# Optimization experiments

Hardware: AMD Instinct MI355X
Metric: run time of the kernel (lower is better)

Reference implementation:

```python
import jax, jax.numpy as jnp
import numpy as np

P = 1024
H = 256
W = 256


def setup_inputs() -> dict:
    key = jax.random.key(0)
    k1, k2, k3, k4, k5, k6 = jax.random.split(key, 6)
    # Means in pixel coordinates, inside the image
    means_2d = jax.random.uniform(k1, (P, 2), dtype=jnp.float32) * jnp.array([W, H], dtype=jnp.float32)
    # Symmetric positive-definite 2x2 covariances packed as (a, b, c) = (cxx, cxy, cyy)
    a = 5.0 + 20.0 * jax.random.uniform(k2, (P,), dtype=jnp.float32)
    c = 5.0 + 20.0 * jax.random.uniform(k3, (P,), dtype=jnp.float32)
    b = (jax.random.uniform(k4, (P,), dtype=jnp.float32) - 0.5) * jnp.sqrt(a * c)  # |b| < 0.5*sqrt(ac) => det > 0
    covs_2d = jnp.stack([a, b, c], axis=-1)
    depth_features = 0.1 + 10.0 * jax.random.uniform(k5, (P,), dtype=jnp.float32)
    color_features = jax.random.uniform(k6, (P, 3), dtype=jnp.float32)
    return {
        "means_2d": means_2d,
        "covs_2d": covs_2d,
        "depth_features": depth_features,
        "color_features": color_features,
        "height": H,
        "width": W,
    }


def reference(means_2d, covs_2d, depth_features, color_features, height, width):
    # Front-to-back ordering by depth (nearest Gaussian composited first)
    order = jnp.argsort(depth_features)
    means = means_2d[order]          # [P,2]
    covs = covs_2d[order]            # [P,3]
    colors = color_features[order]   # [P,3]

    a, b, c = covs[:, 0], covs[:, 1], covs[:, 2]
    det = a * c - b * b
    ia = c / det
    ib = -b / det
    ic = a / det

    xs = jnp.arange(width, dtype=means.dtype) + 0.5   # pixel centers
    ys = jnp.arange(height, dtype=means.dtype) + 0.5
    dx = xs[None, None, :] - means[:, 0][:, None, None]   # [P,1,W]
    dy = ys[None, :, None] - means[:, 1][:, None, None]   # [P,H,1]

    # Mahalanobis distance under inverse 2D covariance (conic)
    q = (ia[:, None, None] * dx * dx
         + 2.0 * ib[:, None, None] * dx * dy
         + ic[:, None, None] * dy * dy)                   # [P,H,W]

    alpha = jnp.minimum(0.99, jnp.exp(-0.5 * q))
    alpha = jnp.where(alpha < 1.0 / 255.0, 0.0, alpha)    # 3DGS skip threshold

    # Exclusive cumulative transmittance along the depth-sorted axis
    T = jnp.cumprod(1.0 - alpha, axis=0)                  # [P,H,W]
    T_excl = jnp.concatenate([jnp.ones_like(T[:1]), T[:-1]], axis=0)
    w = alpha * T_excl                                    # per-Gaussian per-pixel weight

    img = jnp.einsum('pc,phw->chw', colors, w)            # [3,H,W]
    return img
```

## Files before the change

kernel.cpp:

```cpp
#include <hip/hip_runtime.h>


constexpr int P_GAUSS = 1024;
constexpr int IMG_H = 256;
constexpr int IMG_W = 256;
constexpr float Q_GATE = 11.2f;
constexpr float Q_CULL = 11.3f;

__global__ __launch_bounds__(256) void gs_fused(
    const float* __restrict__ means,
    const float* __restrict__ covs,
    const float* __restrict__ depth,
    const float* __restrict__ colors,
    float* __restrict__ out)
{
    __shared__ float g[P_GAUSS * 8];
    __shared__ float sdepth[P_GAUSS];
    __shared__ int   sperm[P_GAUSS];
    __shared__ int   cnt16[16];

    const int tid = threadIdx.y * 16 + threadIdx.x;
    const int wid = tid >> 6;
    const int lane = tid & 63;

    const float tx0 = (float)(blockIdx.x * 16) + 0.5f;
    const float tx1 = tx0 + 15.0f;
    const float ty0 = (float)(blockIdx.y * 16) + 0.5f;
    const float ty1 = ty0 + 15.0f;

    float mx[4], my[4], ca[4], cb[4], cc[4], dp[4], cr[4], cg[4], cbl[4];
    unsigned long long msk[4];
    bool hit[4];
#pragma unroll
    for (int r = 0; r < 4; ++r) {
        const int p = r * 256 + tid;
        const float2 m2 = reinterpret_cast<const float2*>(means)[p];
        mx[r] = m2.x; my[r] = m2.y;
        ca[r] = covs[p * 3 + 0];
        cb[r] = covs[p * 3 + 1];
        cc[r] = covs[p * 3 + 2];
        dp[r] = depth[p];
        cr[r] = colors[p * 3 + 0];
        cg[r] = colors[p * 3 + 1];
        cbl[r] = colors[p * 3 + 2];
        const float rx = sqrtf(Q_CULL * ca[r]);
        const float ry = sqrtf(Q_CULL * cc[r]);
        hit[r] = (mx[r] + rx >= tx0) && (mx[r] - rx <= tx1) &&
                 (my[r] + ry >= ty0) && (my[r] - ry <= ty1);
        msk[r] = __ballot(hit[r]);
        if (lane == 0) cnt16[r * 4 + wid] = __popcll(msk[r]);
    }
    __syncthreads();

    int c16[16];
#pragma unroll
    for (int k = 0; k < 16; ++k) c16[k] = cnt16[k];
    int total = 0;
#pragma unroll
    for (int k = 0; k < 16; ++k) total += c16[k];

#pragma unroll
    for (int r = 0; r < 4; ++r) {
        if (hit[r]) {
            const int key = r * 4 + wid;
            int base = 0;
            for (int k = 0; k < key; ++k) base += c16[k];
            const int slot = base + __popcll(msk[r] & ((1ull << lane) - 1ull));
            float* rec = g + slot * 8;
            rec[0] = mx[r]; rec[1] = my[r];
            rec[2] = ca[r]; rec[3] = cb[r]; rec[4] = cc[r];
            rec[5] = cr[r]; rec[6] = cg[r]; rec[7] = cbl[r];
            sdepth[slot] = dp[r];
        }
    }
    __syncthreads();

    for (int s = tid; s < total; s += 256) {
        const float d = sdepth[s];
        int rank = 0;
        for (int j = 0; j < total; ++j) {
            const float dj = sdepth[j];
            rank += (dj < d || (dj == d && j < s)) ? 1 : 0;
        }
        sperm[rank] = s;
        const float a = g[s * 8 + 2];
        const float b = g[s * 8 + 3];
        const float c = g[s * 8 + 4];
        const float det = a * c - b * b;
        g[s * 8 + 2] = c / det;
        g[s * 8 + 3] = -b / det;
        g[s * 8 + 4] = a / det;
    }
    __syncthreads();

    const float px = tx0 + (float)threadIdx.x;
    const float py = ty0 + (float)threadIdx.y;

    float T = 1.0f;
    float acr = 0.0f, acg = 0.0f, acb = 0.0f;

    const float4* gv = reinterpret_cast<const float4*>(g);
    float4 ra, rb;
    int slN = 0;
    if (total > 0) {
        const int s0 = sperm[0];
        ra = gv[2 * s0]; rb = gv[2 * s0 + 1];
        if (total > 1) slN = sperm[1];
    }
    for (int p = 0; p < total; ++p) {
        const float4 c0 = ra;
        const float4 c1 = rb;
        if (p + 1 < total) { ra = gv[2 * slN]; rb = gv[2 * slN + 1]; }
        if (p + 2 < total) slN = sperm[p + 2];
        const float dx = px - c0.x;
        const float dy = py - c0.y;
        const float q = c0.z * dx * dx + 2.0f * c0.w * (dx * dy) + c1.x * dy * dy;
        if (q < Q_GATE) {
            const float alpha = fminf(0.99f, __expf(-0.5f * q));
            if (alpha >= (1.0f / 255.0f)) {
                const float w = alpha * T;
                acr += w * c1.y;
                acg += w * c1.z;
                acb += w * c1.w;
                T *= (1.0f - alpha);
            }
        }
    }

    const int pix = (blockIdx.y * 16 + threadIdx.y) * IMG_W + (blockIdx.x * 16 + threadIdx.x);
    out[0 * IMG_H * IMG_W + pix] = acr;
    out[1 * IMG_H * IMG_W + pix] = acg;
    out[2 * IMG_H * IMG_W + pix] = acb;
}

extern "C" void kernel_launch(void* const* d_in, const int* in_sizes, int n_in,
                              void* d_out, int out_size, void* d_ws, size_t ws_size,
                              hipStream_t stream) {
    const float* means  = (const float*)d_in[0];
    const float* covs   = (const float*)d_in[1];
    const float* depth  = (const float*)d_in[2];
    const float* colors = (const float*)d_in[3];
    float* out = (float*)d_out;

    gs_fused<<<dim3(IMG_W / 16, IMG_H / 16), dim3(16, 16), 0, stream>>>(
        means, covs, depth, colors, out);
}
```

Before: 16.56 us.

## Stage raw inputs in LDS, vectorize rank sort, scatter records in sorted order

Each block now copies all raw Gaussian inputs into shared memory with coalesced float4 loads instead of strided scalar global loads. The rank-based sort reads depths four at a time, using FLT_MAX padding at the end of the array. Each ranked record is written directly to a depth-sorted buffer, so the permutation array and its indirect lookup are gone and the compositing loop reads records sequentially with a two-deep register prefetch. Shared memory use grows by about 36 KB per block, which may lower occupancy.

```diff
diff --git a/kernel.cpp b/kernel.cpp
--- a/kernel.cpp
+++ b/kernel.cpp
@@ -1,4 +1,5 @@
 #include <hip/hip_runtime.h>
+#include <cfloat>
 
 
 constexpr int P_GAUSS = 1024;
@@ -7,6 +8,12 @@
 constexpr float Q_GATE = 11.2f;
 constexpr float Q_CULL = 11.3f;
 
+constexpr int RAW_MEANS = 0;
+constexpr int RAW_COVS  = 2048;
+constexpr int RAW_DEPTH = 5120;
+constexpr int RAW_COLS  = 6144;
+constexpr int RAW_TOT   = 9216;
+
 __global__ __launch_bounds__(256) void gs_fused(
     const float* __restrict__ means,
     const float* __restrict__ covs,
@@ -14,14 +21,34 @@
     const float* __restrict__ colors,
     float* __restrict__ out)
 {
+    __shared__ float rawbuf[RAW_TOT];
     __shared__ float g[P_GAUSS * 8];
-    __shared__ float sdepth[P_GAUSS];
-    __shared__ int   sperm[P_GAUSS];
+    __shared__ float sdepth[P_GAUSS + 4];
     __shared__ int   cnt16[16];
+
+    float* const g2 = rawbuf;
 
     const int tid = threadIdx.y * 16 + threadIdx.x;
     const int wid = tid >> 6;
     const int lane = tid & 63;
+
+    {
+        float4* rv = reinterpret_cast<float4*>(rawbuf);
+        const float4* mv = reinterpret_cast<const float4*>(means);
+        const float4* cv = reinterpret_cast<const float4*>(covs);
+        const float4* dv = reinterpret_cast<const float4*>(depth);
+        const float4* lv = reinterpret_cast<const float4*>(colors);
+        rv[RAW_MEANS / 4 + tid]       = mv[tid];
+        rv[RAW_MEANS / 4 + 256 + tid] = mv[256 + tid];
+        rv[RAW_COVS / 4 + tid]        = cv[tid];
+        rv[RAW_COVS / 4 + 256 + tid]  = cv[256 + tid];
+        rv[RAW_COVS / 4 + 512 + tid]  = cv[512 + tid];
+        rv[RAW_DEPTH / 4 + tid]       = dv[tid];
+        rv[RAW_COLS / 4 + tid]        = lv[tid];
+        rv[RAW_COLS / 4 + 256 + tid]  = lv[256 + tid];
+        rv[RAW_COLS / 4 + 512 + tid]  = lv[512 + tid];
+    }
+    __syncthreads();
 
     const float tx0 = (float)(blockIdx.x * 16) + 0.5f;
     const float tx1 = tx0 + 15.0f;
@@ -34,15 +61,15 @@
 #pragma unroll
     for (int r = 0; r < 4; ++r) {
         const int p = r * 256 + tid;
-        const float2 m2 = reinterpret_cast<const float2*>(means)[p];
+        const float2 m2 = reinterpret_cast<const float2*>(rawbuf + RAW_MEANS)[p];
         mx[r] = m2.x; my[r] = m2.y;
-        ca[r] = covs[p * 3 + 0];
-        cb[r] = covs[p * 3 + 1];
-        cc[r] = covs[p * 3 + 2];
-        dp[r] = depth[p];
-        cr[r] = colors[p * 3 + 0];
-        cg[r] = colors[p * 3 + 1];
-        cbl[r] = colors[p * 3 + 2];
+        ca[r]  = rawbuf[RAW_COVS + 3 * p + 0];
+        cb[r]  = rawbuf[RAW_COVS + 3 * p + 1];
+        cc[r]  = rawbuf[RAW_COVS + 3 * p + 2];
+        dp[r]  = rawbuf[RAW_DEPTH + p];
+        cr[r]  = rawbuf[RAW_COLS + 3 * p + 0];
+        cg[r]  = rawbuf[RAW_COLS + 3 * p + 1];
+        cbl[r] = rawbuf[RAW_COLS + 3 * p + 2];
         const float rx = sqrtf(Q_CULL * ca[r]);
         const float ry = sqrtf(Q_CULL * cc[r]);
         hit[r] = (mx[r] + rx >= tx0) && (mx[r] - rx <= tx1) &&
@@ -66,30 +93,35 @@
             int base = 0;
             for (int k = 0; k < key; ++k) base += c16[k];
             const int slot = base + __popcll(msk[r] & ((1ull << lane) - 1ull));
-            float* rec = g + slot * 8;
-            rec[0] = mx[r]; rec[1] = my[r];
-            rec[2] = ca[r]; rec[3] = cb[r]; rec[4] = cc[r];
-            rec[5] = cr[r]; rec[6] = cg[r]; rec[7] = cbl[r];
+            float4* rec = reinterpret_cast<float4*>(g + slot * 8);
+            rec[0] = make_float4(mx[r], my[r], ca[r], cb[r]);
+            rec[1] = make_float4(cc[r], cr[r], cg[r], cbl[r]);
             sdepth[slot] = dp[r];
         }
     }
+    if (tid < 4) sdepth[total + tid] = FLT_MAX;
     __syncthreads();
 
+    const int limit4 = (total + 3) >> 2;
     for (int s = tid; s < total; s += 256) {
         const float d = sdepth[s];
         int rank = 0;
-        for (int j = 0; j < total; ++j) {
-            const float dj = sdepth[j];
-            rank += (dj < d || (dj == d && j < s)) ? 1 : 0;
+        const float4* sd4 = reinterpret_cast<const float4*>(sdepth);
+        for (int jj = 0; jj < limit4; ++jj) {
+            const float4 d4 = sd4[jj];
+            const int j = 4 * jj;
+            rank += (d4.x < d || (d4.x == d && j + 0 < s)) ? 1 : 0;
+            rank += (d4.y < d || (d4.y == d && j + 1 < s)) ? 1 : 0;
+            rank += (d4.z < d || (d4.z == d && j + 2 < s)) ? 1 : 0;
+            rank += (d4.w < d || (d4.w == d && j + 3 < s)) ? 1 : 0;
         }
-        sperm[rank] = s;
-        const float a = g[s * 8 + 2];
-        const float b = g[s * 8 + 3];
-        const float c = g[s * 8 + 4];
+        const float4 r0 = reinterpret_cast<const float4*>(g + s * 8)[0];
+        const float4 r1 = reinterpret_cast<const float4*>(g + s * 8)[1];
+        const float a = r0.z, b = r0.w, c = r1.x;
         const float det = a * c - b * b;
-        g[s * 8 + 2] = c / det;
-        g[s * 8 + 3] = -b / det;
-        g[s * 8 + 4] = a / det;
+        float4* dst = reinterpret_cast<float4*>(g2 + rank * 8);
+        dst[0] = make_float4(r0.x, r0.y, c / det, -b / det);
+        dst[1] = make_float4(a / det, r1.y, r1.z, r1.w);
     }
     __syncthreads();
 
@@ -99,19 +131,15 @@
     float T = 1.0f;
     float acr = 0.0f, acg = 0.0f, acb = 0.0f;
 
-    const float4* gv = reinterpret_cast<const float4*>(g);
-    float4 ra, rb;
-    int slN = 0;
-    if (total > 0) {
-        const int s0 = sperm[0];
-        ra = gv[2 * s0]; rb = gv[2 * s0 + 1];
-        if (total > 1) slN = sperm[1];
-    }
+    const float4* gv = reinterpret_cast<const float4*>(g2);
+    float4 A0, B0, A1, B1;
+    if (total > 0) { A0 = gv[0]; B0 = gv[1]; }
+    if (total > 1) { A1 = gv[2]; B1 = gv[3]; }
     for (int p = 0; p < total; ++p) {
-        const float4 c0 = ra;
-        const float4 c1 = rb;
-        if (p + 1 < total) { ra = gv[2 * slN]; rb = gv[2 * slN + 1]; }
-        if (p + 2 < total) slN = sperm[p + 2];
+        const float4 c0 = A0;
+        const float4 c1 = B0;
+        A0 = A1; B0 = B1;
+        if (p + 2 < total) { A1 = gv[2 * p + 4]; B1 = gv[2 * p + 5]; }
         const float dx = px - c0.x;
         const float dy = py - c0.y;
         const float q = c0.z * dx * dx + 2.0f * c0.w * (dx * dy) + c1.x * dy * dy;
```

Result: faster. 15.12 us (-8.7%).
